# Kernel optimization log

Measured on AMD Instinct MI355X. Metric: run time of the kernel, lower is better.

The kernel has to match this reference:

```python
import jax, jax.numpy as jnp
import numpy as np

STEPS = 3
TOP_N = 2
ROUTE_TEMP = 1.5


def setup_inputs() -> dict:
    key = jax.random.key(0)
    ks = jax.random.split(key, 7)
    B, H, W, C = 16, 112, 112, 128
    heads, dh = 2, 64
    hd = heads * dh  # 128
    K = 4
    s_in = 0.02  # keep activations well-scaled through 3 steps
    x = jax.random.normal(ks[0], (B, H, W, C), dtype=jnp.float32)
    Wk = jax.random.normal(ks[1], (C, hd), dtype=jnp.float32) * s_in
    Wv = jax.random.normal(ks[2], (C, hd), dtype=jnp.float32) * s_in
    q = jax.random.normal(ks[3], (heads, dh), dtype=jnp.float32) * 0.1
    Wmlp = jax.random.normal(ks[4], (hd, K), dtype=jnp.float32) * 0.1
    Wb = jax.random.normal(ks[5], (K, C, C), dtype=jnp.float32) * (1.0 / np.sqrt(C))
    alpha = jnp.zeros((), dtype=jnp.float32)  # attn_log_alpha
    return {"x": x, "Wk": Wk, "Wv": Wv, "q": q, "Wmlp": Wmlp, "Wb": Wb, "alpha": alpha}


def _router(x, Wk, Wv, q, Wmlp):
    # AttnPoolRouter: 1x1 conv K/V, single-query-per-head softmax attention pool.
    B, H, W, C = x.shape
    heads, dh = q.shape
    L = H * W
    k = jnp.einsum('bhwc,ce->bhwe', x, Wk).reshape(B, L, heads, dh)  # [B,L,h,d]
    v = jnp.einsum('bhwc,ce->bhwe', x, Wv).reshape(B, L, heads, dh)
    scores = jnp.einsum('hd,blhd->bhl', q, k) / jnp.sqrt(jnp.asarray(dh, x.dtype))
    attn = jax.nn.softmax(scores, axis=-1)                            # [B,h,L]
    pooled = jnp.einsum('bhl,blhd->bhd', attn, v).reshape(B, heads * dh)
    logits = pooled @ Wmlp                                            # [B,K]
    attn_map = attn.mean(axis=1).reshape(B, H, W, 1)                  # [B,H,W,1]
    return logits, attn_map


def reference(x, Wk, Wv, q, Wmlp, Wb, alpha):
    B, H, W, C = x.shape
    K = Wmlp.shape[1]
    scale = jnp.asarray(H * W, x.dtype)
    a = jax.nn.softplus(alpha)
    for _ in range(STEPS):
        logits, attn_map = _router(x, Wk, Wv, q, Wmlp)
        weights = jax.nn.softmax(logits / ROUTE_TEMP, axis=-1)        # [B,K]
        _, top_idx = jax.lax.top_k(weights, TOP_N)                    # [B,top_n]
        top_mask = jax.nn.one_hot(top_idx, K, dtype=weights.dtype).sum(axis=1)
        wm = weights * top_mask
        ws = wm / (wm.sum(axis=-1, keepdims=True) + 1e-9)
        # straight-through: forward = renormalized top-n, gradient flows to full softmax
        wst = ws + jax.lax.stop_gradient(weights - ws)                # [B,K]
        x_mod = x * (1.0 + attn_map * scale * a)                      # [B,H,W,C]
        # all K branch 1x1 convs, combined by straight-through weights
        x = jnp.einsum('bhwc,kcd,bk->bhwd', x_mod, Wb, wst)
    return x
```

## Files before the change

kernel.cpp:

```cpp
#include <hip/hip_runtime.h>
#include <hip/hip_bf16.h>
#include <cstdint>

#define NB 16
#define NC 128
#define NL 12544
#define NHD 128
#define NK 4
#define ROWS (NB*NL)
#define CH 128
#define PCH2 98

typedef unsigned short ushort_t;
typedef __attribute__((ext_vector_type(8))) short bf16x8;
typedef __attribute__((ext_vector_type(4))) float f32x4;

__device__ __forceinline__ float bf2f(unsigned u){
  union { unsigned i; float f; } v; v.i = u << 16; return v.f;
}
__device__ __forceinline__ ushort_t f2bf(float f){
  unsigned u = __float_as_uint(f);
  return (ushort_t)((u + 0x7FFFu + ((u >> 16) & 1u)) >> 16);
}

__global__ void __launch_bounds__(256,4) k_pass1(const float* __restrict__ x,
    const float* __restrict__ Wk, const float* __restrict__ q,
    float* __restrict__ sraw, float* __restrict__ pm, float* __restrict__ pS,
    float* __restrict__ pP){
  __shared__ __align__(16) ushort_t xs[CH*NC];
  __shared__ float sqk[NC*2];
  __shared__ float shs0[CH], shs1[CH];
  __shared__ float red[8];
  __shared__ float pmerge[256];
  int b = blockIdx.x / PCH2, chunk = blockIdx.x % PCH2;
  int l0 = chunk*CH;
  int t = threadIdx.x, lane = t & 63, wave = t >> 6;
  int hi = lane >> 4, n16 = lane & 15;

  {
    const float* src = x + ((size_t)b*NL + l0)*NC;
    #pragma unroll
    for (int i = 0; i < 16; ++i){
      int idx = i*1024 + t*4;
      int row = idx >> 7;
      float4 v = *(const float4*)(src + idx);
      unsigned p0 = (unsigned)f2bf(v.x) | ((unsigned)f2bf(v.y) << 16);
      unsigned p1 = (unsigned)f2bf(v.z) | ((unsigned)f2bf(v.w) << 16);
      *(uint2*)((char*)xs + ((idx*2) ^ ((row & 7) << 4))) = make_uint2(p0, p1);
    }
  }
  {
    int c = t >> 1, h = t & 1;
    float s = 0.f;
    #pragma unroll 8
    for (int d = 0; d < 64; ++d) s += Wk[c*NHD + h*64 + d] * q[h*64 + d];
    sqk[c*2 + h] = s * 0.125f;
  }
  __syncthreads();

  bf16x8 qfv[4];
  #pragma unroll
  for (int kk = 0; kk < 4; ++kk)
    #pragma unroll
    for (int j = 0; j < 8; ++j){
      int k = kk*32 + hi*8 + j;
      qfv[kk][j] = (n16 < 2) ? (short)f2bf(sqk[k*2 + n16]) : (short)0;
    }

  #pragma unroll
  for (int rt2 = 0; rt2 < 2; ++rt2){
    int rt = wave*2 + rt2;
    f32x4 acc = (f32x4){0.f,0.f,0.f,0.f};
    #pragma unroll
    for (int kk = 0; kk < 4; ++kk){
      int row = rt*16 + n16;
      int k = kk*32 + hi*8;
      bf16x8 a = *(const bf16x8*)((const char*)xs + ((row*256 + k*2) ^ ((row & 7) << 4)));
      acc = __builtin_amdgcn_mfma_f32_16x16x32_bf16(a, qfv[kk], acc, 0, 0, 0);
    }
    if (n16 < 2){
      float* dst = n16 ? shs1 : shs0;
      #pragma unroll
      for (int r = 0; r < 4; ++r) dst[rt*16 + hi*4 + r] = acc[r];
    }
  }
  __syncthreads();

  float s0 = -3.4e38f, s1 = -3.4e38f;
  if (t < 128){
    s0 = shs0[t]; s1 = shs1[t];
    sraw[((size_t)b*2+0)*NL + l0 + t] = s0;
    sraw[((size_t)b*2+1)*NL + l0 + t] = s1;
  }
  float m0 = s0, m1 = s1;
  #pragma unroll
  for (int mk = 32; mk; mk >>= 1){ m0 = fmaxf(m0, __shfl_xor(m0, mk)); m1 = fmaxf(m1, __shfl_xor(m1, mk)); }
  if (lane == 0 && wave < 2){ red[wave] = m0; red[2+wave] = m1; }
  __syncthreads();
  float M0 = fmaxf(red[0], red[1]), M1 = fmaxf(red[2], red[3]);
  float e0 = 0.f, e1 = 0.f;
  if (t < 128){ e0 = __expf(s0 - M0); e1 = __expf(s1 - M1); shs0[t] = e0; shs1[t] = e1; }
  float t0 = e0, t1 = e1;
  #pragma unroll
  for (int mk = 32; mk; mk >>= 1){ t0 += __shfl_xor(t0, mk); t1 += __shfl_xor(t1, mk); }
  if (lane == 0 && wave < 2){ red[4+wave] = t0; red[6+wave] = t1; }
  __syncthreads();
  if (t == 0){
    pm[(b*2+0)*PCH2 + chunk] = M0; pm[(b*2+1)*PCH2 + chunk] = M1;
    pS[(b*2+0)*PCH2 + chunk] = red[4]+red[5];
    pS[(b*2+1)*PCH2 + chunk] = red[6]+red[7];
  }

  int h = t >> 7, half = (t >> 6) & 1, cp = t & 63;
  const float* es = h ? shs1 : shs0;
  float a0 = 0.f, a1 = 0.f;
  #pragma unroll 4
  for (int i = 0; i < 64; ++i){
    int l = half*64 + i;
    float e = es[l];
    unsigned u = *(const unsigned*)((const char*)xs + ((l*256 + 4*cp) ^ ((l & 7) << 4)));
    a0 += e * bf2f(u & 0xffffu);
    a1 += e * bf2f(u >> 16);
  }
  __syncthreads();
  if (half){ pmerge[h*128 + cp*2] = a0; pmerge[h*128 + cp*2 + 1] = a1; }
  __syncthreads();
  if (!half){
    a0 += pmerge[h*128 + cp*2];
    a1 += pmerge[h*128 + cp*2 + 1];
    float2 w; w.x = a0; w.y = a1;
    *(float2*)&pP[(((size_t)b*PCH2 + chunk)*2 + h)*NC + 2*cp] = w;
  }
}

template<typename XIN, typename XOUT, bool STATS>
__global__ void __launch_bounds__(256,2) k_gemm(const XIN* __restrict__ xin,
    const float* __restrict__ Wk, const float* __restrict__ q,
    const float* __restrict__ alpha, const float* __restrict__ Wv,
    const float* __restrict__ Wmlp, const float* __restrict__ Wb,
    float* __restrict__ sraw,
    const float* __restrict__ pmR, const float* __restrict__ pSR, const float* __restrict__ pPR,
    float* __restrict__ pmW, float* __restrict__ pSW, float* __restrict__ pPW,
    XOUT* __restrict__ xout){
  __shared__ __align__(16) ushort_t lA[CH*NC];
  __shared__ __align__(16) ushort_t lB[NC*NHD];
  __shared__ float sqk[NC*2];
  __shared__ float w98[2][PCH2];
  __shared__ float pxs[2][NC];
  __shared__ float vpool[NHD];
  __shared__ float wts[NK];
  __shared__ float mSh[4];
  __shared__ float shmod[CH];
  __shared__ float shs0[CH], shs1[CH];
  __shared__ float red[8];
  __shared__ float pacc[4][2][NC];
  int b = blockIdx.x >> 5, part = blockIdx.x & 31;
  int t = threadIdx.x, lane = t & 63, wave = t >> 6;

  float av = alpha[0];
  float sp = (av > 20.f) ? av : log1pf(__expf(av));
  float sa = (float)NL * sp * 0.5f;

  if (STATS){
    int c = t >> 1, h = t & 1;
    float s = 0.f;
    #pragma unroll 8
    for (int d = 0; d < 64; ++d) s += Wk[c*NHD + h*64 + d] * q[h*64 + d];
    sqk[c*2 + h] = s * 0.125f;
  }
  if (wave < 2){
    int h = wave;
    const float* pmh = pmR + (b*2+h)*PCH2;
    const float* pSh = pSR + (b*2+h)*PCH2;
    float m = -3.4e38f;
    for (int j = lane; j < PCH2; j += 64) m = fmaxf(m, pmh[j]);
    #pragma unroll
    for (int mk = 32; mk; mk >>= 1) m = fmaxf(m, __shfl_xor(m, mk));
    float S = 0.f;
    for (int j = lane; j < PCH2; j += 64) S += pSh[j] * __expf(pmh[j] - m);
    #pragma unroll
    for (int mk = 32; mk; mk >>= 1) S += __shfl_xor(S, mk);
    for (int j = lane; j < PCH2; j += 64) w98[h][j] = __expf(pmh[j] - m);
    if (lane == 0){ mSh[h] = m; mSh[2+h] = 1.f/S; }
  }
  __syncthreads();
  {
    int h = t >> 7, c = t & 127;
    float s = 0.f;
    #pragma unroll 2
    for (int j = 0; j < PCH2; ++j) s += pPR[(((size_t)b*PCH2 + j)*2 + h)*NC + c] * w98[h][j];
    pxs[h][c] = s * mSh[2+h];
  }
  __syncthreads();
  if (t < NHD){
    int h = t >> 6, d = t & 63;
    float s = 0.f;
    for (int c = 0; c < NC; ++c) s += pxs[h][c] * Wv[c*NHD + h*64 + d];
    vpool[t] = s;
  }
  __syncthreads();
  if (t < 64){
    float lg = 0.f;
    if (lane < 4){
      for (int e = 0; e < NHD; ++e) lg += vpool[e] * Wmlp[e*NK + lane];
      lg *= (1.0f/1.5f);
    }
    float m01 = fmaxf(lg, __shfl_xor(lg, 1));
    float mall = fmaxf(m01, __shfl_xor(m01, 2));
    float e = __expf(lg - mall);
    float s01 = e + __shfl_xor(e, 1);
    float sall = s01 + __shfl_xor(s01, 2);
    if (lane < 4) wts[lane] = e / sall;
  }
  __syncthreads();
  {
    float w0 = wts[0], w1 = wts[1], w2 = wts[2], w3 = wts[3];
    for (int idx = t; idx < NC*NC; idx += 256){
      int c = idx >> 7, d = idx & 127;
      const float* wb = Wb + (size_t)c*NC + d;
      float v = w0*wb[0] + w1*wb[NC*NC] + w2*wb[2*NC*NC] + w3*wb[3*NC*NC];
      *(ushort_t*)((char*)lB + ((d*256 + c*2) ^ ((d & 7) << 4))) = f2bf(v);
    }
  }

  int trow = lane & 15, kg = lane >> 4, r0 = wave*32;
  for (int ci = part; ci < PCH2; ci += 32){
    int l0 = ci*CH;
    const float* s0p = sraw + ((size_t)b*2 + 0)*NL + l0;
    const float* s1p = sraw + ((size_t)b*2 + 1)*NL + l0;
    __syncthreads();

    if constexpr (sizeof(XIN) == 4){
      const float* src = (const float*)xin + ((size_t)b*NL + l0)*NC;
      #pragma unroll
      for (int i = 0; i < 16; ++i){
        int idx = i*1024 + t*4;
        int row = idx >> 7;
        float4 v = *(const float4*)(src + idx);
        unsigned p0 = (unsigned)f2bf(v.x) | ((unsigned)f2bf(v.y) << 16);
        unsigned p1 = (unsigned)f2bf(v.z) | ((unsigned)f2bf(v.w) << 16);
        *(uint2*)((char*)lA + ((idx*2) ^ ((row & 7) << 4))) = make_uint2(p0, p1);
      }
    } else {
      const ushort_t* src = (const ushort_t*)xin + ((size_t)b*NL + l0)*NC;
      #pragma unroll
      for (int i = 0; i < 8; ++i){
        int idx = i*2048 + t*8;
        int row = idx >> 7;
        uint4 v = *(const uint4*)(src + idx);
        *(uint4*)((char*)lA + ((idx*2) ^ ((row & 7) << 4))) = v;
      }
    }
    if (t < CH)
      shmod[t] = 1.f + sa*(__expf(s0p[t]-mSh[0])*mSh[2] + __expf(s1p[t]-mSh[1])*mSh[3]);
    __syncthreads();

    f32x4 acc[2][8];
    #pragma unroll
    for (int m = 0; m < 2; ++m)
      #pragma unroll
      for (int n = 0; n < 8; ++n) acc[m][n] = (f32x4){0.f,0.f,0.f,0.f};
    #pragma unroll
    for (int kk = 0; kk < 4; ++kk){
      int k = kk*32 + kg*8;
      int ra0 = r0 + trow, ra1 = r0 + 16 + trow;
      bf16x8 a0 = *(const bf16x8*)((const char*)lA + ((ra0*256 + k*2) ^ ((ra0 & 7) << 4)));
      bf16x8 a1 = *(const bf16x8*)((const char*)lA + ((ra1*256 + k*2) ^ ((ra1 & 7) << 4)));
      #pragma unroll
      for (int nt = 0; nt < 8; ++nt){
        int col = nt*16 + trow;
        bf16x8 bf = *(const bf16x8*)((const char*)lB + ((col*256 + k*2) ^ ((col & 7) << 4)));
        acc[0][nt] = __builtin_amdgcn_mfma_f32_16x16x32_bf16(a0, bf, acc[0][nt], 0, 0, 0);
        acc[1][nt] = __builtin_amdgcn_mfma_f32_16x16x32_bf16(a1, bf, acc[1][nt], 0, 0, 0);
      }
    }

    float md[2][4];
    #pragma unroll
    for (int m = 0; m < 2; ++m)
      #pragma unroll
      for (int r = 0; r < 4; ++r) md[m][r] = shmod[r0 + m*16 + kg*4 + r];

    size_t base = ((size_t)b*NL + l0)*NC;
    #pragma unroll
    for (int m = 0; m < 2; ++m)
      #pragma unroll
      for (int nt = 0; nt < 8; ++nt)
        #pragma unroll
        for (int r = 0; r < 4; ++r){
          int row = r0 + m*16 + kg*4 + r;
          int col = nt*16 + trow;
          float v = acc[m][nt][r] * md[m][r];
          if constexpr (sizeof(XOUT) == 4) ((float*)xout)[base + (size_t)row*NC + col] = v;
          else                             ((ushort_t*)xout)[base + (size_t)row*NC + col] = f2bf(v);
        }

    if (STATS){
      float wq0[8], wq1[8];
      #pragma unroll
      for (int nt = 0; nt < 8; ++nt){
        wq0[nt] = sqk[(nt*16 + trow)*2 + 0];
        wq1[nt] = sqk[(nt*16 + trow)*2 + 1];
      }
      #pragma unroll
      for (int m = 0; m < 2; ++m)
        #pragma unroll
        for (int r = 0; r < 4; ++r){
          float p0 = 0.f, p1 = 0.f;
          #pragma unroll
          for (int nt = 0; nt < 8; ++nt){ float v = acc[m][nt][r]; p0 += v*wq0[nt]; p1 += v*wq1[nt]; }
          #pragma unroll
          for (int mk = 1; mk < 16; mk <<= 1){ p0 += __shfl_xor(p0, mk); p1 += __shfl_xor(p1, mk); }
          int idx = m*4 + r;
          if (trow == idx){
            int row = r0 + m*16 + kg*4 + r;
            shs0[row] = p0 * md[m][r]; shs1[row] = p1 * md[m][r];
          }
        }
      __syncthreads();

      float s0 = -3.4e38f, s1 = -3.4e38f;
      if (t < 128){
        s0 = shs0[t]; s1 = shs1[t];
        sraw[((size_t)b*2+0)*NL + l0 + t] = s0;
        sraw[((size_t)b*2+1)*NL + l0 + t] = s1;
      }
      float m0 = s0, m1 = s1;
      #pragma unroll
      for (int mk = 32; mk; mk >>= 1){ m0 = fmaxf(m0, __shfl_xor(m0, mk)); m1 = fmaxf(m1, __shfl_xor(m1, mk)); }
      if (lane == 0 && wave < 2){ red[wave] = m0; red[2+wave] = m1; }
      __syncthreads();
      float M0 = fmaxf(red[0], red[1]), M1 = fmaxf(red[2], red[3]);
      float e0 = 0.f, e1 = 0.f;
      if (t < 128){ e0 = __expf(s0 - M0); e1 = __expf(s1 - M1); shs0[t] = e0; shs1[t] = e1; }
      float t0 = e0, t1 = e1;
      #pragma unroll
      for (int mk = 32; mk; mk >>= 1){ t0 += __shfl_xor(t0, mk); t1 += __shfl_xor(t1, mk); }
      if (lane == 0 && wave < 2){ red[4+wave] = t0; red[6+wave] = t1; }
      __syncthreads();
      if (t == 0){
        pmW[(b*2+0)*PCH2 + ci] = M0; pmW[(b*2+1)*PCH2 + ci] = M1;
        pSW[(b*2+0)*PCH2 + ci] = red[4]+red[5];
        pSW[(b*2+1)*PCH2 + ci] = red[6]+red[7];
      }

      float ea0[2][4], ea1[2][4];
      #pragma unroll
      for (int m = 0; m < 2; ++m)
        #pragma unroll
        for (int r = 0; r < 4; ++r){
          int row = r0 + m*16 + kg*4 + r;
          ea0[m][r] = shs0[row] * md[m][r]; ea1[m][r] = shs1[row] * md[m][r];
        }
      #pragma unroll
      for (int nt = 0; nt < 8; ++nt){
        float p0 = 0.f, p1 = 0.f;
        #pragma unroll
        for (int m = 0; m < 2; ++m)
          #pragma unroll
          for (int r = 0; r < 4; ++r){
            p0 += ea0[m][r]*acc[m][nt][r];
            p1 += ea1[m][r]*acc[m][nt][r];
          }
        p0 += __shfl_xor(p0, 16); p0 += __shfl_xor(p0, 32);
        p1 += __shfl_xor(p1, 16); p1 += __shfl_xor(p1, 32);
        int col = nt*16 + trow;
        if (kg == 0) pacc[wave][0][col] = p0;
        if (kg == 1) pacc[wave][1][col] = p1;
      }
      __syncthreads();
      {
        int h = t >> 7, c = t & 127;
        pPW[(((size_t)b*PCH2 + ci)*2 + h)*NC + c] =
          pacc[0][h][c] + pacc[1][h][c] + pacc[2][h][c] + pacc[3][h][c];
      }
    }
  }
}

extern "C" void kernel_launch(void* const* d_in, const int* in_sizes, int n_in,
                              void* d_out, int out_size, void* d_ws, size_t ws_size,
                              hipStream_t stream){
  const float* x0   = (const float*)d_in[0];
  const float* Wk   = (const float*)d_in[1];
  const float* Wv   = (const float*)d_in[2];
  const float* q    = (const float*)d_in[3];
  const float* Wmlp = (const float*)d_in[4];
  const float* Wb   = (const float*)d_in[5];
  const float* alpha= (const float*)d_in[6];
  float* out = (float*)d_out;

  char* ws = (char*)d_ws;
  float* sraw = (float*)ws;
  float* pmA  = sraw + (size_t)NB*2*NL;
  float* pSA  = pmA + NB*2*PCH2;
  float* pmB  = pSA + NB*2*PCH2;
  float* pSB  = pmB + NB*2*PCH2;
  float* pPA  = pSB + NB*2*PCH2;
  float* pPB  = pPA + (size_t)NB*PCH2*2*NC;
  char* endf  = (char*)(pPB + (size_t)NB*PCH2*2*NC);
  size_t xoff = ((size_t)(endf - ws) + 255) & ~(size_t)255;
  ushort_t* xb = (ushort_t*)(ws + xoff);
  bool big = ws_size >= xoff + (size_t)ROWS*NC*2;

  k_pass1<<<NB*PCH2, 256, 0, stream>>>(x0, Wk, q, sraw, pmA, pSA, pPA);

  dim3 g(NB*32);
  if (big){
    k_gemm<float,    ushort_t, true ><<<g, 256, 0, stream>>>(x0, Wk, q, alpha, Wv, Wmlp, Wb,
        sraw, pmA, pSA, pPA, pmB, pSB, pPB, xb);
    k_gemm<ushort_t, ushort_t, true ><<<g, 256, 0, stream>>>(xb, Wk, q, alpha, Wv, Wmlp, Wb,
        sraw, pmB, pSB, pPB, pmA, pSA, pPA, xb);
    k_gemm<ushort_t, float,    false><<<g, 256, 0, stream>>>(xb, Wk, q, alpha, Wv, Wmlp, Wb,
        sraw, pmA, pSA, pPA, pmB, pSB, pPB, out);
  } else {
    k_gemm<float, float, true ><<<g, 256, 0, stream>>>(x0, Wk, q, alpha, Wv, Wmlp, Wb,
        sraw, pmA, pSA, pPA, pmB, pSB, pPB, out);
    k_gemm<float, float, true ><<<g, 256, 0, stream>>>(out, Wk, q, alpha, Wv, Wmlp, Wb,
        sraw, pmB, pSB, pPB, pmA, pSA, pPA, out);
    k_gemm<float, float, false><<<g, 256, 0, stream>>>(out, Wk, q, alpha, Wv, Wmlp, Wb,
        sraw, pmA, pSA, pPA, pmB, pSB, pPB, out);
  }
}
```

Measured before the change: 400.4 us.

## Load A fragments directly to registers, cut LDS, raise occupancy and grid

```diff
diff --git a/kernel.cpp b/kernel.cpp
--- a/kernel.cpp
+++ b/kernel.cpp
@@ -10,6 +10,7 @@
 #define ROWS (NB*NL)
 #define CH 128
 #define PCH2 98
+#define GPB 49
 
 typedef unsigned short ushort_t;
 typedef __attribute__((ext_vector_type(8))) short bf16x8;
@@ -134,7 +135,7 @@
 }
 
 template<typename XIN, typename XOUT, bool STATS>
-__global__ void __launch_bounds__(256,2) k_gemm(const XIN* __restrict__ xin,
+__global__ void __launch_bounds__(256,4) k_gemm(const XIN* __restrict__ xin,
     const float* __restrict__ Wk, const float* __restrict__ q,
     const float* __restrict__ alpha, const float* __restrict__ Wv,
     const float* __restrict__ Wmlp, const float* __restrict__ Wb,
@@ -142,20 +143,22 @@
     const float* __restrict__ pmR, const float* __restrict__ pSR, const float* __restrict__ pPR,
     float* __restrict__ pmW, float* __restrict__ pSW, float* __restrict__ pPW,
     XOUT* __restrict__ xout){
-  __shared__ __align__(16) ushort_t lA[CH*NC];
   __shared__ __align__(16) ushort_t lB[NC*NHD];
   __shared__ float sqk[NC*2];
-  __shared__ float w98[2][PCH2];
-  __shared__ float pxs[2][NC];
-  __shared__ float vpool[NHD];
-  __shared__ float wts[NK];
   __shared__ float mSh[4];
-  __shared__ float shmod[CH];
   __shared__ float shs0[CH], shs1[CH];
   __shared__ float red[8];
-  __shared__ float pacc[4][2][NC];
-  int b = blockIdx.x >> 5, part = blockIdx.x & 31;
+  __shared__ __align__(16) char ubuf[4096];
+  float (*w98)[PCH2]   = (float(*)[PCH2])ubuf;
+  float (*pxs)[NC]     = (float(*)[NC])(ubuf + 2*PCH2*4);
+  float* vpool         = (float*)(ubuf + (2*PCH2 + 2*NC)*4);
+  float* wts           = vpool + NHD;
+  float (*pacc)[2][NC] = (float(*)[2][NC])ubuf;
+
+  int wg = ((blockIdx.x & 7) * (NB*GPB/8)) + (blockIdx.x >> 3);
+  int b = wg / GPB, part = wg % GPB;
   int t = threadIdx.x, lane = t & 63, wave = t >> 6;
+  int trow = lane & 15, kg = lane >> 4, r0 = wave*32;
 
   float av = alpha[0];
   float sp = (av > 20.f) ? av : log1pf(__expf(av));
@@ -187,7 +190,7 @@
   {
     int h = t >> 7, c = t & 127;
     float s = 0.f;
-    #pragma unroll 2
+    #pragma unroll 8
     for (int j = 0; j < PCH2; ++j) s += pPR[(((size_t)b*PCH2 + j)*2 + h)*NC + c] * w98[h][j];
     pxs[h][c] = s * mSh[2+h];
   }
@@ -195,6 +198,7 @@
   if (t < NHD){
     int h = t >> 6, d = t & 63;
     float s = 0.f;
+    #pragma unroll 4
     for (int c = 0; c < NC; ++c) s += pxs[h][c] * Wv[c*NHD + h*64 + d];
     vpool[t] = s;
   }
@@ -222,38 +226,50 @@
       *(ushort_t*)((char*)lB + ((d*256 + c*2) ^ ((d & 7) << 4))) = f2bf(v);
     }
   }
-
-  int trow = lane & 15, kg = lane >> 4, r0 = wave*32;
-  for (int ci = part; ci < PCH2; ci += 32){
+  __syncthreads();
+
+  float am0 = mSh[0], am1 = mSh[1], ai0 = mSh[2], ai1 = mSh[3];
+  const float* sr0 = sraw + ((size_t)b*2 + 0)*NL;
+  const float* sr1 = sraw + ((size_t)b*2 + 1)*NL;
+
+  for (int ci = part; ci < PCH2; ci += GPB){
     int l0 = ci*CH;
-    const float* s0p = sraw + ((size_t)b*2 + 0)*NL + l0;
-    const float* s1p = sraw + ((size_t)b*2 + 1)*NL + l0;
-    __syncthreads();
-
+    int ga0 = l0 + r0 + trow, ga1 = ga0 + 16;
+
+    bf16x8 af0[4], af1[4];
     if constexpr (sizeof(XIN) == 4){
-      const float* src = (const float*)xin + ((size_t)b*NL + l0)*NC;
-      #pragma unroll
-      for (int i = 0; i < 16; ++i){
-        int idx = i*1024 + t*4;
-        int row = idx >> 7;
-        float4 v = *(const float4*)(src + idx);
-        unsigned p0 = (unsigned)f2bf(v.x) | ((unsigned)f2bf(v.y) << 16);
-        unsigned p1 = (unsigned)f2bf(v.z) | ((unsigned)f2bf(v.w) << 16);
-        *(uint2*)((char*)lA + ((idx*2) ^ ((row & 7) << 4))) = make_uint2(p0, p1);
+      const float* p0 = (const float*)xin + ((size_t)b*NL + ga0)*NC + kg*8;
+      const float* p1 = (const float*)xin + ((size_t)b*NL + ga1)*NC + kg*8;
+      #pragma unroll
+      for (int kk = 0; kk < 4; ++kk){
+        float4 u0 = *(const float4*)(p0 + kk*32), u1 = *(const float4*)(p0 + kk*32 + 4);
+        float4 v0 = *(const float4*)(p1 + kk*32), v1 = *(const float4*)(p1 + kk*32 + 4);
+        af0[kk][0] = (short)f2bf(u0.x); af0[kk][1] = (short)f2bf(u0.y);
+        af0[kk][2] = (short)f2bf(u0.z); af0[kk][3] = (short)f2bf(u0.w);
+        af0[kk][4] = (short)f2bf(u1.x); af0[kk][5] = (short)f2bf(u1.y);
+        af0[kk][6] = (short)f2bf(u1.z); af0[kk][7] = (short)f2bf(u1.w);
+        af1[kk][0] = (short)f2bf(v0.x); af1[kk][1] = (short)f2bf(v0.y);
+        af1[kk][2] = (short)f2bf(v0.z); af1[kk][3] = (short)f2bf(v0.w);
+        af1[kk][4] = (short)f2bf(v1.x); af1[kk][5] = (short)f2bf(v1.y);
+        af1[kk][6] = (short)f2bf(v1.z); af1[kk][7] = (short)f2bf(v1.w);
       }
     } else {
-      const ushort_t* src = (const ushort_t*)xin + ((size_t)b*NL + l0)*NC;
-      #pragma unroll
-      for (int i = 0; i < 8; ++i){
-        int idx = i*2048 + t*8;
-        int row = idx >> 7;
-        uint4 v = *(const uint4*)(src + idx);
-        *(uint4*)((char*)lA + ((idx*2) ^ ((row & 7) << 4))) = v;
-      }
-    }
-    if (t < CH)
-      shmod[t] = 1.f + sa*(__expf(s0p[t]-mSh[0])*mSh[2] + __expf(s1p[t]-mSh[1])*mSh[3]);
-    __syncthreads();
+      const ushort_t* p0 = (const ushort_t*)xin + ((size_t)b*NL + ga0)*NC + kg*8;
+      const ushort_t* p1 = (const ushort_t*)xin + ((size_t)b*NL + ga1)*NC + kg*8;
+      #pragma unroll
+      for (int kk = 0; kk < 4; ++kk){
+        af0[kk] = *(const bf16x8*)(p0 + kk*32);
+        af1[kk] = *(const bf16x8*)(p1 + kk*32);
+      }
+    }
+    float md[2][4];
+    #pragma unroll
+    for (int m = 0; m < 2; ++m)
+      #pragma unroll
+      for (int r = 0; r < 4; ++r){
+        int rw = l0 + r0 + m*16 + kg*4 + r;
+        md[m][r] = 1.f + sa*(__expf(sr0[rw]-am0)*ai0 + __expf(sr1[rw]-am1)*ai1);
+      }
 
     f32x4 acc[2][8];
     #pragma unroll
@@ -263,52 +279,27 @@
     #pragma unroll
     for (int kk = 0; kk < 4; ++kk){
       int k = kk*32 + kg*8;
-      int ra0 = r0 + trow, ra1 = r0 + 16 + trow;
-      bf16x8 a0 = *(const bf16x8*)((const char*)lA + ((ra0*256 + k*2) ^ ((ra0 & 7) << 4)));
-      bf16x8 a1 = *(const bf16x8*)((const char*)lA + ((ra1*256 + k*2) ^ ((ra1 & 7) << 4)));
       #pragma unroll
       for (int nt = 0; nt < 8; ++nt){
         int col = nt*16 + trow;
         bf16x8 bf = *(const bf16x8*)((const char*)lB + ((col*256 + k*2) ^ ((col & 7) << 4)));
-        acc[0][nt] = __builtin_amdgcn_mfma_f32_16x16x32_bf16(a0, bf, acc[0][nt], 0, 0, 0);
-        acc[1][nt] = __builtin_amdgcn_mfma_f32_16x16x32_bf16(a1, bf, acc[1][nt], 0, 0, 0);
-      }
-    }
-
-    float md[2][4];
-    #pragma unroll
-    for (int m = 0; m < 2; ++m)
-      #pragma unroll
-      for (int r = 0; r < 4; ++r) md[m][r] = shmod[r0 + m*16 + kg*4 + r];
-
-    size_t base = ((size_t)b*NL + l0)*NC;
-    #pragma unroll
-    for (int m = 0; m < 2; ++m)
-      #pragma unroll
-      for (int nt = 0; nt < 8; ++nt)
-        #pragma unroll
-        for (int r = 0; r < 4; ++r){
-          int row = r0 + m*16 + kg*4 + r;
-          int col = nt*16 + trow;
-          float v = acc[m][nt][r] * md[m][r];
-          if constexpr (sizeof(XOUT) == 4) ((float*)xout)[base + (size_t)row*NC + col] = v;
-          else                             ((ushort_t*)xout)[base + (size_t)row*NC + col] = f2bf(v);
-        }
+        acc[0][nt] = __builtin_amdgcn_mfma_f32_16x16x32_bf16(af0[kk], bf, acc[0][nt], 0, 0, 0);
+        acc[1][nt] = __builtin_amdgcn_mfma_f32_16x16x32_bf16(af1[kk], bf, acc[1][nt], 0, 0, 0);
+      }
+    }
 
     if (STATS){
-      float wq0[8], wq1[8];
-      #pragma unroll
-      for (int nt = 0; nt < 8; ++nt){
-        wq0[nt] = sqk[(nt*16 + trow)*2 + 0];
-        wq1[nt] = sqk[(nt*16 + trow)*2 + 1];
-      }
       #pragma unroll
       for (int m = 0; m < 2; ++m)
         #pragma unroll
         for (int r = 0; r < 4; ++r){
           float p0 = 0.f, p1 = 0.f;
           #pragma unroll
-          for (int nt = 0; nt < 8; ++nt){ float v = acc[m][nt][r]; p0 += v*wq0[nt]; p1 += v*wq1[nt]; }
+          for (int nt = 0; nt < 8; ++nt){
+            float v = acc[m][nt][r];
+            p0 += v*sqk[(nt*16 + trow)*2 + 0];
+            p1 += v*sqk[(nt*16 + trow)*2 + 1];
+          }
           #pragma unroll
           for (int mk = 1; mk < 16; mk <<= 1){ p0 += __shfl_xor(p0, mk); p1 += __shfl_xor(p1, mk); }
           int idx = m*4 + r;
@@ -374,7 +365,22 @@
         pPW[(((size_t)b*PCH2 + ci)*2 + h)*NC + c] =
           pacc[0][h][c] + pacc[1][h][c] + pacc[2][h][c] + pacc[3][h][c];
       }
-    }
+      __syncthreads();
+    }
+
+    size_t base = ((size_t)b*NL + l0)*NC;
+    #pragma unroll
+    for (int m = 0; m < 2; ++m)
+      #pragma unroll
+      for (int nt = 0; nt < 8; ++nt)
+        #pragma unroll
+        for (int r = 0; r < 4; ++r){
+          int row = r0 + m*16 + kg*4 + r;
+          int col = nt*16 + trow;
+          float v = acc[m][nt][r] * md[m][r];
+          if constexpr (sizeof(XOUT) == 4) ((float*)xout)[base + (size_t)row*NC + col] = v;
+          else                             ((ushort_t*)xout)[base + (size_t)row*NC + col] = f2bf(v);
+        }
   }
 }
 
@@ -405,7 +411,7 @@
 
   k_pass1<<<NB*PCH2, 256, 0, stream>>>(x0, Wk, q, sraw, pmA, pSA, pPA);
 
-  dim3 g(NB*32);
+  dim3 g(NB*GPB);
   if (big){
     k_gemm<float,    ushort_t, true ><<<g, 256, 0, stream>>>(x0, Wk, q, alpha, Wv, Wmlp, Wb,
         sraw, pmA, pSA, pPA, pmB, pSB, pPB, xb);
```

Result: slower. 527.5 us (+31.8%).
